# Kernel tuning notes

Hardware: AMD Instinct MI355X
Metric: run time of the kernel (lower is better)

Reference implementation:

```python
import jax, jax.numpy as jnp
import numpy as np

B, S, E, H = 4, 1024, 1024, 16
D = E // H  # head_dim = 64
SCALE = float(np.sqrt(D))


def setup_inputs() -> dict:
    key = jax.random.key(0)
    ks = jax.random.split(key, 12)
    lim = 1.0 / np.sqrt(E)  # torch nn.Linear default init range

    def lin(kw, kb):
        W = jax.random.uniform(kw, (E, E), jnp.float32, -lim, lim)
        b = jax.random.uniform(kb, (E,), jnp.float32, -lim, lim)
        return W, b

    W0, b0 = lin(ks[0], ks[1])
    W1, b1 = lin(ks[2], ks[3])
    W2, b2 = lin(ks[4], ks[5])
    Wv, bv = lin(ks[6], ks[7])
    Wo, bo = lin(ks[8], ks[9])
    A = jax.random.normal(ks[10], (D, D, D), jnp.float32)  # torch.randn core tensor
    x = jax.random.normal(ks[11], (B, S, E), jnp.float32)
    return {"x": x, "W0": W0, "b0": b0, "W1": W1, "b1": b1, "W2": W2, "b2": b2,
            "Wv": Wv, "bv": bv, "Wo": Wo, "bo": bo, "A": A}


def _heads(h):
    # (B,S,E) -> (B,H,S,D)
    return h.reshape(B, S, H, D).transpose(0, 2, 1, 3)


def reference(x, W0, b0, W1, b1, W2, b2, Wv, bv, Wo, bo, A):
    p0 = _heads(x @ W0.T + b0)
    p1 = _heads(x @ W1.T + b1)
    p2 = _heads(x @ W2.T + b2)
    # N=3 multilinear attention score: third projection is contracted over its
    # own sequence index k (faithful to the original einsum construction).
    logits = jnp.einsum('acd,bhia,bhjc,bhkd->bhij', A, p0, p1, p2,
                        optimize=True) / SCALE  # (B,H,S,S)
    attn = jax.nn.softmax(logits, axis=-1)  # dropout inactive (eval / p=0)
    v = _heads(x @ Wv.T + bv)
    values = jnp.einsum('bhij,bhjd->bhid', attn, v)  # (B,H,S,D)
    values = values.transpose(0, 2, 1, 3).reshape(B, S, E)
    out = values @ Wo.T + bo
    return out, attn
```

## Files before the change

kernel.cpp:

```cpp
#include <hip/hip_runtime.h>
#include <hip/hip_bf16.h>
#include <cstddef>

#define B_ 4
#define S_ 1024
#define E_ 1024
#define H_ 16
#define D_ 64
#define BH_ (B_*H_)

typedef __attribute__((ext_vector_type(8))) short short8;
typedef __attribute__((ext_vector_type(4))) float f32x4;
typedef __attribute__((ext_vector_type(4))) unsigned short us4;
typedef unsigned short u16;

__device__ inline u16 f2b(float x) {
    return __builtin_bit_cast(u16, __float2bfloat16(x));
}
__device__ inline float b2f(u16 u) {
    return __bfloat162float(__builtin_bit_cast(__hip_bfloat16, u));
}
__device__ inline void splitf(float x, u16& h, u16& l) {
    h = f2b(x); l = f2b(x - b2f(h));
}

__device__ inline void split_one(const float* __restrict__ in,
                                 u16* __restrict__ oh, u16* __restrict__ ol, int i)
{
    float4 v = ((const float4*)in)[i];
    us4 h, l;
    splitf(v.x, ((u16*)&h)[0], ((u16*)&l)[0]);
    splitf(v.y, ((u16*)&h)[1], ((u16*)&l)[1]);
    splitf(v.z, ((u16*)&h)[2], ((u16*)&l)[2]);
    splitf(v.w, ((u16*)&h)[3], ((u16*)&l)[3]);
    ((us4*)oh)[i] = h;
    ((us4*)ol)[i] = l;
}

__device__ inline void conv_one(const float* __restrict__ in,
                                u16* __restrict__ ob, int i)
{
    float4 v = ((const float4*)in)[i];
    us4 h;
    ((u16*)&h)[0] = f2b(v.x); ((u16*)&h)[1] = f2b(v.y);
    ((u16*)&h)[2] = f2b(v.z); ((u16*)&h)[3] = f2b(v.w);
    ((us4*)ob)[i] = h;
}

__global__ __launch_bounds__(256) void prep(
    const float* __restrict__ x, const float* __restrict__ W0,
    const float* __restrict__ W1, const float* __restrict__ Wv,
    const float* __restrict__ Wo, float* __restrict__ xsum_p,
    u16* __restrict__ xh, u16* __restrict__ xl,
    u16* __restrict__ w0h, u16* __restrict__ w0l,
    u16* __restrict__ w1h, u16* __restrict__ w1l,
    u16* __restrict__ wvb, u16* __restrict__ wob)
{
    int bid = blockIdx.x, tid = threadIdx.x;
    if (bid < 4096) {
        split_one(x, xh, xl, bid * 256 + tid);
    } else if (bid < 5120) {
        split_one(W0, w0h, w0l, (bid - 4096) * 256 + tid);
    } else if (bid < 6144) {
        split_one(W1, w1h, w1l, (bid - 5120) * 256 + tid);
    } else if (bid < 7168) {
        conv_one(Wv, wvb, (bid - 6144) * 256 + tid);
    } else if (bid < 8192) {
        conv_one(Wo, wob, (bid - 7168) * 256 + tid);
    } else {
        int p = bid - 8192;
        int kb = p & 3, b = (p >> 2) & 3, ch = p >> 4;
        int k = kb * 256 + tid;
        const float* base = x + ((size_t)(b * S_ + ch * 64)) * E_ + k;
        float s = 0.f;
#pragma unroll 8
        for (int j = 0; j < 64; ++j) s += base[(size_t)j * E_];
        xsum_p[(ch * 4 + b) * E_ + k] = s;
    }
}

__global__ __launch_bounds__(256) void t2k_M(
    const float* __restrict__ W2, const float* __restrict__ b2v,
    const float* __restrict__ xsum_p, const float* __restrict__ A,
    u16* __restrict__ MTh, u16* __restrict__ MTl)
{
    int h = blockIdx.x, b = blockIdx.y, tid = threadIdx.x;
    __shared__ float xs[1024];
    __shared__ float t2s[64];

#pragma unroll
    for (int j = 0; j < 4; ++j) {
        int k = j * 256 + tid;
        float s = 0.f;
#pragma unroll
        for (int c = 0; c < 16; ++c) s += xsum_p[(c * 4 + b) * E_ + k];
        xs[k] = s;
    }
    __syncthreads();

    int w = tid >> 6, lane = tid & 63;
    for (int nn = w; nn < 64; nn += 4) {
        int n = h * 64 + nn;
        const float* wr = W2 + (size_t)n * E_;
        float s = 0.f;
#pragma unroll
        for (int t = 0; t < 16; ++t) s = fmaf(wr[t * 64 + lane], xs[t * 64 + lane], s);
#pragma unroll
        for (int off = 1; off < 64; off <<= 1) s += __shfl_xor(s, off, 64);
        if (lane == 0) t2s[nn] = s + 1024.0f * b2v[n];
    }
    __syncthreads();

    int bh = b * H_ + h;
    int c = tid & 63;
    int a0 = (tid >> 6) * 16;
    for (int a = a0; a < a0 + 16; ++a) {
        float s = 0.f;
        const float* Ap = A + ((size_t)a * 64 + c) * 64;
#pragma unroll 8
        for (int d = 0; d < 64; ++d) s = fmaf(Ap[d], t2s[d], s);
        u16 hh, ll; splitf(s * 0.125f, hh, ll);
        MTh[(size_t)bh * 4096 + c * 64 + a] = hh;
        MTl[(size_t)bh * 4096 + c * 64 + a] = ll;
    }
}

__device__ void qp1_body(
    const u16* __restrict__ Xh, const u16* __restrict__ Xl,
    const u16* __restrict__ W0h_, const u16* __restrict__ W0l_,
    const u16* __restrict__ W1h_, const u16* __restrict__ W1l_,
    const float* __restrict__ bias0, const float* __restrict__ bias1,
    const u16* __restrict__ MTh, const u16* __restrict__ MTl,
    u16* __restrict__ qh, u16* __restrict__ ql,
    u16* __restrict__ p1h, u16* __restrict__ p1l,
    int bm, int bn, char* smem)
{
    const int K = 1024;
    u16* Xs_h  = (u16*)smem;
    u16* Xs_l  = Xs_h + 128 * 40;
    u16* W0s_h = Xs_l + 128 * 40;
    u16* W0s_l = W0s_h + 64 * 40;
    u16* W1s_h = W0s_l + 64 * 40;
    u16* W1s_l = W1s_h + 64 * 40;
    u16* Cs_h  = (u16*)smem;
    u16* Cs_l  = Cs_h + 128 * 72;

    const int tid = threadIdx.x;
    const int w = tid >> 6, lane = tid & 63;
    const int waveM = w & 1, waveN = w >> 1;
    const int quad = lane >> 4, l16 = lane & 15;

    const int xrow = tid >> 1, xko = (tid & 1) * 16;
    const int wrow = tid >> 2, wko = (tid & 3) * 8;

    const u16* xh_g  = Xh  + (size_t)(bm * 128 + xrow) * K + xko;
    const u16* xl_g  = Xl  + (size_t)(bm * 128 + xrow) * K + xko;
    const u16* w0h_g = W0h_ + (size_t)(bn * 64 + wrow) * K + wko;
    const u16* w0l_g = W0l_ + (size_t)(bn * 64 + wrow) * K + wko;
    const u16* w1h_g = W1h_ + (size_t)(bn * 64 + wrow) * K + wko;
    const u16* w1l_g = W1l_ + (size_t)(bn * 64 + wrow) * K + wko;

    f32x4 acc0[4][2] = {};
    f32x4 acc1[4][2] = {};

    for (int k0 = 0; k0 < K; k0 += 32) {
        uint4 xa = *(const uint4*)(xh_g + k0);
        uint4 xb = *(const uint4*)(xh_g + k0 + 8);
        uint4 xc = *(const uint4*)(xl_g + k0);
        uint4 xd = *(const uint4*)(xl_g + k0 + 8);
        uint4 w0a = *(const uint4*)(w0h_g + k0);
        uint4 w0c = *(const uint4*)(w0l_g + k0);
        uint4 w1a = *(const uint4*)(w1h_g + k0);
        uint4 w1c = *(const uint4*)(w1l_g + k0);
        __syncthreads();
        *(uint4*)&Xs_h[xrow * 40 + xko]     = xa;
        *(uint4*)&Xs_h[xrow * 40 + xko + 8] = xb;
        *(uint4*)&Xs_l[xrow * 40 + xko]     = xc;
        *(uint4*)&Xs_l[xrow * 40 + xko + 8] = xd;
        *(uint4*)&W0s_h[wrow * 40 + wko] = w0a;
        *(uint4*)&W0s_l[wrow * 40 + wko] = w0c;
        *(uint4*)&W1s_h[wrow * 40 + wko] = w1a;
        *(uint4*)&W1s_l[wrow * 40 + wko] = w1c;
        __syncthreads();

        short8 ah[4], al[4], b0h[2], b0l[2], b1h[2], b1l[2];
#pragma unroll
        for (int mt = 0; mt < 4; ++mt) {
            int r = (waveM * 64 + mt * 16 + l16) * 40 + quad * 8;
            ah[mt] = *(short8*)&Xs_h[r];
            al[mt] = *(short8*)&Xs_l[r];
        }
#pragma unroll
        for (int nt = 0; nt < 2; ++nt) {
            int r = (waveN * 32 + nt * 16 + l16) * 40 + quad * 8;
            b0h[nt] = *(short8*)&W0s_h[r];
            b0l[nt] = *(short8*)&W0s_l[r];
            b1h[nt] = *(short8*)&W1s_h[r];
            b1l[nt] = *(short8*)&W1s_l[r];
        }
#pragma unroll
        for (int mt = 0; mt < 4; ++mt)
#pragma unroll
            for (int nt = 0; nt < 2; ++nt) {
                acc0[mt][nt] = __builtin_amdgcn_mfma_f32_16x16x32_bf16(ah[mt], b0h[nt], acc0[mt][nt], 0, 0, 0);
                acc1[mt][nt] = __builtin_amdgcn_mfma_f32_16x16x32_bf16(ah[mt], b1h[nt], acc1[mt][nt], 0, 0, 0);
                acc0[mt][nt] = __builtin_amdgcn_mfma_f32_16x16x32_bf16(ah[mt], b0l[nt], acc0[mt][nt], 0, 0, 0);
                acc1[mt][nt] = __builtin_amdgcn_mfma_f32_16x16x32_bf16(ah[mt], b1l[nt], acc1[mt][nt], 0, 0, 0);
                acc0[mt][nt] = __builtin_amdgcn_mfma_f32_16x16x32_bf16(al[mt], b0h[nt], acc0[mt][nt], 0, 0, 0);
                acc1[mt][nt] = __builtin_amdgcn_mfma_f32_16x16x32_bf16(al[mt], b1h[nt], acc1[mt][nt], 0, 0, 0);
            }
    }

    const int bh = (bm >> 3) * H_ + bn;

#pragma unroll
    for (int mt = 0; mt < 4; ++mt)
#pragma unroll
        for (int nt = 0; nt < 2; ++nt)
#pragma unroll
            for (int r = 0; r < 4; ++r) {
                int m = bm * 128 + waveM * 64 + mt * 16 + quad * 4 + r;
                int n = bn * 64 + waveN * 32 + nt * 16 + l16;
                float val = acc1[mt][nt][r] + bias1[n];
                int s = m & 1023, c = n & 63;
                size_t addr = ((size_t)bh * S_ + s) * 64 + c;
                u16 hh, ll; splitf(val, hh, ll);
                p1h[addr] = hh; p1l[addr] = ll;
            }

    __syncthreads();
#pragma unroll
    for (int mt = 0; mt < 4; ++mt)
#pragma unroll
        for (int nt = 0; nt < 2; ++nt)
#pragma unroll
            for (int r = 0; r < 4; ++r) {
                int i = waveM * 64 + mt * 16 + quad * 4 + r;
                int a = waveN * 32 + nt * 16 + l16;
                float val = acc0[mt][nt][r] + bias0[bn * 64 + a];
                u16 hh, ll; splitf(val, hh, ll);
                Cs_h[i * 72 + a] = hh;
                Cs_l[i * 72 + a] = ll;
            }
    __syncthreads();

    const u16* MTh_b = MTh + (size_t)bh * 4096;
    const u16* MTl_b = MTl + (size_t)bh * 4096;
    f32x4 qacc[4][2] = {};
#pragma unroll
    for (int ch = 0; ch < 2; ++ch) {
        short8 mh[2], ml[2];
#pragma unroll
        for (int nt = 0; nt < 2; ++nt) {
            int c = waveN * 32 + nt * 16 + l16;
            mh[nt] = *(const short8*)&MTh_b[c * 64 + ch * 32 + quad * 8];
            ml[nt] = *(const short8*)&MTl_b[c * 64 + ch * 32 + quad * 8];
        }
#pragma unroll
        for (int mt = 0; mt < 4; ++mt) {
            int rr = (waveM * 64 + mt * 16 + l16) * 72 + ch * 32 + quad * 8;
            short8 ca = *(short8*)&Cs_h[rr];
            short8 cl = *(short8*)&Cs_l[rr];
#pragma unroll
            for (int nt = 0; nt < 2; ++nt) {
                qacc[mt][nt] = __builtin_amdgcn_mfma_f32_16x16x32_bf16(ca, mh[nt], qacc[mt][nt], 0, 0, 0);
                qacc[mt][nt] = __builtin_amdgcn_mfma_f32_16x16x32_bf16(ca, ml[nt], qacc[mt][nt], 0, 0, 0);
                qacc[mt][nt] = __builtin_amdgcn_mfma_f32_16x16x32_bf16(cl, mh[nt], qacc[mt][nt], 0, 0, 0);
            }
        }
    }
#pragma unroll
    for (int mt = 0; mt < 4; ++mt)
#pragma unroll
        for (int nt = 0; nt < 2; ++nt)
#pragma unroll
            for (int r = 0; r < 4; ++r) {
                int s = (bm & 7) * 128 + waveM * 64 + mt * 16 + quad * 4 + r;
                int c = waveN * 32 + nt * 16 + l16;
                size_t addr = ((size_t)bh * S_ + s) * 64 + c;
                u16 hh, ll; splitf(qacc[mt][nt][r], hh, ll);
                qh[addr] = hh; ql[addr] = ll;
            }
}

__device__ void plain128_body(
    const u16* __restrict__ Xb, const u16* __restrict__ Wb,
    const float* __restrict__ bias, u16* __restrict__ outB,
    float* __restrict__ outF, int mode, int bm, int bn, char* smem)
{
    const int K = 1024;
    u16* Xs = (u16*)smem;
    u16* Ws = Xs + 128 * 40;

    const int tid = threadIdx.x;
    const int w = tid >> 6, lane = tid & 63;
    const int waveM = w & 1, waveN = w >> 1;
    const int quad = lane >> 4, l16 = lane & 15;
    const int row = tid >> 1, ko = (tid & 1) * 16;

    const u16* xg = Xb + (size_t)(bm * 128 + row) * K + ko;
    const u16* wg = Wb + (size_t)(bn * 128 + row) * K + ko;

    f32x4 acc[4][4] = {};

    for (int k0 = 0; k0 < K; k0 += 32) {
        uint4 xa = *(const uint4*)(xg + k0);
        uint4 xb = *(const uint4*)(xg + k0 + 8);
        uint4 wa = *(const uint4*)(wg + k0);
        uint4 wb = *(const uint4*)(wg + k0 + 8);
        __syncthreads();
        *(uint4*)&Xs[row * 40 + ko]     = xa;
        *(uint4*)&Xs[row * 40 + ko + 8] = xb;
        *(uint4*)&Ws[row * 40 + ko]     = wa;
        *(uint4*)&Ws[row * 40 + ko + 8] = wb;
        __syncthreads();

        short8 af[4], bf_[4];
#pragma unroll
        for (int mt = 0; mt < 4; ++mt)
            af[mt] = *(short8*)&Xs[(waveM * 64 + mt * 16 + l16) * 40 + quad * 8];
#pragma unroll
        for (int nt = 0; nt < 4; ++nt)
            bf_[nt] = *(short8*)&Ws[(waveN * 64 + nt * 16 + l16) * 40 + quad * 8];
#pragma unroll
        for (int mt = 0; mt < 4; ++mt)
#pragma unroll
            for (int nt = 0; nt < 4; ++nt)
                acc[mt][nt] = __builtin_amdgcn_mfma_f32_16x16x32_bf16(af[mt], bf_[nt], acc[mt][nt], 0, 0, 0);
    }

#pragma unroll
    for (int mt = 0; mt < 4; ++mt)
#pragma unroll
        for (int nt = 0; nt < 4; ++nt)
#pragma unroll
            for (int r = 0; r < 4; ++r) {
                int m = bm * 128 + waveM * 64 + mt * 16 + quad * 4 + r;
                int n = bn * 128 + waveN * 64 + nt * 16 + l16;
                float val = acc[mt][nt][r] + bias[n];
                if (mode == 0) {
                    int b = m >> 10, s = m & 1023, h = n >> 6, c = n & 63;
                    outB[((size_t)((b * H_ + h) * 64 + c)) * S_ + s] = f2b(val);
                } else {
                    outF[(size_t)m * 1024 + n] = val;
                }
            }
}

__global__ __launch_bounds__(256) void gemm_mid(
    const u16* __restrict__ xh, const u16* __restrict__ xl,
    const u16* __restrict__ w0h, const u16* __restrict__ w0l,
    const u16* __restrict__ w1h, const u16* __restrict__ w1l,
    const float* __restrict__ b0, const float* __restrict__ b1,
    const u16* __restrict__ MTh, const u16* __restrict__ MTl,
    u16* __restrict__ qh, u16* __restrict__ ql,
    u16* __restrict__ p1h, u16* __restrict__ p1l,
    const u16* __restrict__ wvb, const float* __restrict__ bv,
    u16* __restrict__ vT)
{
    __shared__ __align__(16) char smem[40960];
    int bid0 = blockIdx.x;
    if (bid0 < 512) {
        int bid = (bid0 & 7) * 64 + (bid0 >> 3);
        qp1_body(xh, xl, w0h, w0l, w1h, w1l, b0, b1, MTh, MTl,
                 qh, ql, p1h, p1l, bid & 31, bid >> 5, smem);
    } else {
        int b2 = bid0 - 512;
        b2 = (b2 & 7) * 32 + (b2 >> 3);
        plain128_body(xh, wvb, bv, vT, nullptr, 0, b2 & 31, b2 >> 5, smem);
    }
}

__global__ __launch_bounds__(256) void gemm_fin(
    const u16* __restrict__ values, const u16* __restrict__ wob,
    const float* __restrict__ bo, float* __restrict__ out)
{
    __shared__ __align__(16) char smem[20480];
    plain128_body(values, wob, bo, nullptr, out, 1, blockIdx.x, blockIdx.y, smem);
}

__global__ __launch_bounds__(512) void logits_softmax_pv(
    const u16* __restrict__ qh, const u16* __restrict__ ql,
    const u16* __restrict__ p1h, const u16* __restrict__ p1l,
    const u16* __restrict__ vT, float* __restrict__ attn,
    u16* __restrict__ values)
{
    int bh = blockIdx.x, i0 = blockIdx.y * 32;
    int b = bh >> 4, h = bh & 15;
    int tid = threadIdx.x, w = tid >> 6, lane = tid & 63;
    int quad = lane >> 4, l16 = lane & 15;
    int wg = w >> 2, wj = w & 3;

    __shared__ __align__(16) char sm[56320];
    u16* qhs  = (u16*)sm;
    u16* qls  = (u16*)(sm + 4608);
    u16* p1hs = (u16*)(sm + 9216);
    u16* p1ls = (u16*)(sm + 27648);
    float* redm = (float*)(sm + 55296);
    float* reds = (float*)(sm + 55808);
    u16* Ps  = (u16*)sm;
    u16* vs_ = (u16*)(sm + 18432);

    {
        int row = tid >> 4, c0 = (tid & 15) * 4;
        size_t g = ((size_t)bh * S_ + i0 + row) * 64 + c0;
        *(us4*)&qhs[row * 72 + c0] = *(const us4*)&qh[g];
        *(us4*)&qls[row * 72 + c0] = *(const us4*)&ql[g];
    }

    const int jl = tid >> 3, c0s = (tid & 7) * 8;
    const size_t gp = ((size_t)bh * S_ + jl) * 64 + c0s;

    uint4 rha = *(const uint4*)&p1h[gp];
    uint4 rla = *(const uint4*)&p1l[gp];
    *(uint4*)&p1hs[jl * 72 + c0s] = rha;
    *(uint4*)&p1ls[jl * 72 + c0s] = rla;
    uint4 rh1 = *(const uint4*)&p1h[gp + 4096];
    uint4 rl1 = *(const uint4*)&p1l[gp + 4096];
    __syncthreads();

    short8 ah[2], al[2];
#pragma unroll
    for (int ch = 0; ch < 2; ++ch) {
        ah[ch] = *(short8*)&qhs[(wg * 16 + l16) * 72 + ch * 32 + quad * 8];
        al[ch] = *(short8*)&qls[(wg * 16 + l16) * 72 + ch * 32 + quad * 8];
    }

    f32x4 L[16];
    for (int t = 0; t < 16; ++t) {
        int cur = t & 1;
        uint4 rh2, rl2;
        if (t < 14) {
            size_t gn = gp + (size_t)(t + 2) * 4096;
            rh2 = *(const uint4*)&p1h[gn];
            rl2 = *(const uint4*)&p1l[gn];
        }
        int jr = wj * 16 + l16;
        const u16* Hb = &p1hs[cur * 4608 + jr * 72];
        const u16* Lb = &p1ls[cur * 4608 + jr * 72];
        short8 bh0 = *(const short8*)(Hb + quad * 8);
        short8 bh1 = *(const short8*)(Hb + 32 + quad * 8);
        short8 bl0 = *(const short8*)(Lb + quad * 8);
        short8 bl1 = *(const short8*)(Lb + 32 + quad * 8);
        f32x4 a = {};
        a = __builtin_amdgcn_mfma_f32_16x16x32_bf16(ah[0], bh0, a, 0, 0, 0);
        a = __builtin_amdgcn_mfma_f32_16x16x32_bf16(ah[1], bh1, a, 0, 0, 0);
        a = __builtin_amdgcn_mfma_f32_16x16x32_bf16(ah[0], bl0, a, 0, 0, 0);
        a = __builtin_amdgcn_mfma_f32_16x16x32_bf16(ah[1], bl1, a, 0, 0, 0);
        a = __builtin_amdgcn_mfma_f32_16x16x32_bf16(al[0], bh0, a, 0, 0, 0);
        a = __builtin_amdgcn_mfma_f32_16x16x32_bf16(al[1], bh1, a, 0, 0, 0);
        L[t] = a;
        if (t < 15) {
            *(uint4*)&p1hs[(1 - cur) * 4608 + jl * 72 + c0s] = rh1;
            *(uint4*)&p1ls[(1 - cur) * 4608 + jl * 72 + c0s] = rl1;
            if (t < 14) { rh1 = rh2; rl1 = rl2; }
            __syncthreads();
        }
    }

    float mrow[4], srow[4];
#pragma unroll
    for (int r = 0; r < 4; ++r) {
        float m = L[0][r];
#pragma unroll
        for (int t = 1; t < 16; ++t) m = fmaxf(m, L[t][r]);
#pragma unroll
        for (int off = 1; off < 16; off <<= 1) m = fmaxf(m, __shfl_xor(m, off, 64));
        mrow[r] = m;
    }
    if (l16 == 0)
#pragma unroll
        for (int r = 0; r < 4; ++r) redm[wj * 32 + wg * 16 + quad * 4 + r] = mrow[r];
    __syncthreads();
#pragma unroll
    for (int r = 0; r < 4; ++r) {
        int rowg = wg * 16 + quad * 4 + r;
        float m = fmaxf(fmaxf(redm[0 * 32 + rowg], redm[1 * 32 + rowg]),
                        fmaxf(redm[2 * 32 + rowg], redm[3 * 32 + rowg]));
        float s = 0.f;
#pragma unroll
        for (int t = 0; t < 16; ++t) { L[t][r] = __expf(L[t][r] - m); s += L[t][r]; }
#pragma unroll
        for (int off = 1; off < 16; off <<= 1) s += __shfl_xor(s, off, 64);
        srow[r] = s;
    }
    if (l16 == 0)
#pragma unroll
        for (int r = 0; r < 4; ++r) reds[wj * 32 + wg * 16 + quad * 4 + r] = srow[r];
    __syncthreads();
#pragma unroll
    for (int r = 0; r < 4; ++r) {
        int rowg = wg * 16 + quad * 4 + r;
        float inv = 1.0f / (reds[0 * 32 + rowg] + reds[1 * 32 + rowg] +
                            reds[2 * 32 + rowg] + reds[3 * 32 + rowg]);
        float* arow = attn + ((size_t)bh * S_ + i0 + rowg) * S_;
#pragma unroll
        for (int t = 0; t < 16; ++t) {
            float p = L[t][r] * inv;
            L[t][r] = p;
            __builtin_nontemporal_store(p, &arow[t * 64 + wj * 16 + l16]);
        }
    }

    const int dv = tid >> 3, jc = (tid & 7) * 8;
    const size_t gv = (size_t)(bh * 64 + dv) * S_;
    uint4 rv0 = *(const uint4*)&vT[gv + jc];
    uint4 rv1 = *(const uint4*)&vT[gv + 64 + jc];

    f32x4 acc_pv = {};
    const int d = wj * 16 + l16;
    for (int tt = 0; tt < 8; ++tt) {
        int cur = tt & 1;
        u16* Pb = Ps + cur * 4608;
        u16* Vb = vs_ + cur * 9216;
#pragma unroll
        for (int r = 0; r < 4; ++r) {
            int pr = (wg * 16 + quad * 4 + r) * 72 + wj * 16 + l16;
            Pb[pr]        = f2b(L[2 * tt][r]);
            Pb[2304 + pr] = f2b(L[2 * tt + 1][r]);
        }
        *(uint4*)&Vb[dv * 72 + jc]        = rv0;
        *(uint4*)&Vb[4608 + dv * 72 + jc] = rv1;
        __syncthreads();
        if (tt < 7) {
            rv0 = *(const uint4*)&vT[gv + (size_t)(2 * tt + 2) * 64 + jc];
            rv1 = *(const uint4*)&vT[gv + (size_t)(2 * tt + 3) * 64 + jc];
        }
#pragma unroll
        for (int tp = 0; tp < 2; ++tp)
#pragma unroll
            for (int cc = 0; cc < 64; cc += 32) {
                short8 af = *(short8*)&Pb[tp * 2304 + (wg * 16 + l16) * 72 + cc + quad * 8];
                short8 bf = *(short8*)&vs_[cur * 9216 + tp * 4608 + d * 72 + cc + quad * 8];
                acc_pv = __builtin_amdgcn_mfma_f32_16x16x32_bf16(af, bf, acc_pv, 0, 0, 0);
            }
    }
#pragma unroll
    for (int r = 0; r < 4; ++r) {
        int i = i0 + wg * 16 + quad * 4 + r;
        values[((size_t)(b * S_ + i)) * E_ + h * 64 + d] = f2b(acc_pv[r]);
    }
}

extern "C" void kernel_launch(void* const* d_in, const int* in_sizes, int n_in,
                              void* d_out, int out_size, void* d_ws, size_t ws_size,
                              hipStream_t stream)
{
    const float* x  = (const float*)d_in[0];
    const float* W0 = (const float*)d_in[1];
    const float* b0 = (const float*)d_in[2];
    const float* W1 = (const float*)d_in[3];
    const float* b1 = (const float*)d_in[4];
    const float* W2 = (const float*)d_in[5];
    const float* b2 = (const float*)d_in[6];
    const float* Wv = (const float*)d_in[7];
    const float* bv = (const float*)d_in[8];
    const float* Wo = (const float*)d_in[9];
    const float* bo = (const float*)d_in[10];
    const float* A  = (const float*)d_in[11];

    float* out  = (float*)d_out;
    float* attn = out + (size_t)B_ * S_ * E_;

    u16* xh  = (u16*)d_ws;
    u16* xl  = xh + 4194304;
    u16* w0h = xl + 4194304;
    u16* w0l = w0h + 1048576;
    u16* w1h = w0l + 1048576;
    u16* w1l = w1h + 1048576;
    u16* p1h = w1l + 1048576;
    u16* p1l = p1h + 4194304;
    u16* qh  = p1l + 4194304;
    u16* ql  = qh + 4194304;
    u16* vT  = ql + 4194304;
    u16* values = vT + 4194304;
    u16* MTh = values + 4194304;
    u16* MTl = MTh + 262144;
    u16* wob = MTl + 262144;
    float* xsum_p = (float*)p1h;
    u16* wvb = values;

    prep<<<8448, 256, 0, stream>>>(x, W0, W1, Wv, Wo, xsum_p,
                                   xh, xl, w0h, w0l, w1h, w1l, wvb, wob);
    t2k_M<<<dim3(16, 4), 256, 0, stream>>>(W2, b2, xsum_p, A, MTh, MTl);

    gemm_mid<<<768, 256, 0, stream>>>(xh, xl, w0h, w0l, w1h, w1l,
                                      b0, b1, MTh, MTl, qh, ql, p1h, p1l,
                                      wvb, bv, vT);

    logits_softmax_pv<<<dim3(64, 32), 512, 0, stream>>>(qh, ql, p1h, p1l, vT, attn, values);

    gemm_fin<<<dim3(32, 8), 256, 0, stream>>>(values, wob, bo, out);
}
```

Measured before the change: 546.3 us.

## Double query rows per block in fused logits-softmax-PV kernel to halve K/V reloads

Each block of the attention kernel now handles 64 query rows instead of 32, with each wave computing two 16-row sub-tiles. The p1 (key-side) and vT tiles streamed through shared memory are shared by twice as many rows, halving their global loads and LDS staging per output. The PV loop is restructured into 16 single-tile steps. In exchange the grid halves to 1024 blocks, register pressure roughly doubles (two 16-entry logit arrays held per thread), and occupancy may drop.

```diff
diff --git a/kernel.cpp b/kernel.cpp
--- a/kernel.cpp
+++ b/kernel.cpp
@@ -385,27 +385,27 @@
     const u16* __restrict__ vT, float* __restrict__ attn,
     u16* __restrict__ values)
 {
-    int bh = blockIdx.x, i0 = blockIdx.y * 32;
+    int bh = blockIdx.x, i0 = blockIdx.y * 64;
     int b = bh >> 4, h = bh & 15;
     int tid = threadIdx.x, w = tid >> 6, lane = tid & 63;
     int quad = lane >> 4, l16 = lane & 15;
     int wg = w >> 2, wj = w & 3;
 
-    __shared__ __align__(16) char sm[56320];
+    __shared__ __align__(16) char sm[57344];
     u16* qhs  = (u16*)sm;
-    u16* qls  = (u16*)(sm + 4608);
-    u16* p1hs = (u16*)(sm + 9216);
-    u16* p1ls = (u16*)(sm + 27648);
+    u16* qls  = (u16*)(sm + 9216);
+    u16* p1hs = (u16*)(sm + 18432);
+    u16* p1ls = (u16*)(sm + 36864);
     float* redm = (float*)(sm + 55296);
-    float* reds = (float*)(sm + 55808);
+    float* reds = (float*)(sm + 56320);
     u16* Ps  = (u16*)sm;
     u16* vs_ = (u16*)(sm + 18432);
 
     {
-        int row = tid >> 4, c0 = (tid & 15) * 4;
+        int row = tid >> 3, c0 = (tid & 7) * 8;
         size_t g = ((size_t)bh * S_ + i0 + row) * 64 + c0;
-        *(us4*)&qhs[row * 72 + c0] = *(const us4*)&qh[g];
-        *(us4*)&qls[row * 72 + c0] = *(const us4*)&ql[g];
+        *(uint4*)&qhs[row * 72 + c0] = *(const uint4*)&qh[g];
+        *(uint4*)&qls[row * 72 + c0] = *(const uint4*)&ql[g];
     }
 
     const int jl = tid >> 3, c0s = (tid & 7) * 8;
@@ -419,14 +419,17 @@
     uint4 rl1 = *(const uint4*)&p1l[gp + 4096];
     __syncthreads();
 
-    short8 ah[2], al[2];
-#pragma unroll
-    for (int ch = 0; ch < 2; ++ch) {
-        ah[ch] = *(short8*)&qhs[(wg * 16 + l16) * 72 + ch * 32 + quad * 8];
-        al[ch] = *(short8*)&qls[(wg * 16 + l16) * 72 + ch * 32 + quad * 8];
-    }
-
-    f32x4 L[16];
+    short8 ah[2][2], al[2][2];
+#pragma unroll
+    for (int rb = 0; rb < 2; ++rb)
+#pragma unroll
+        for (int ch = 0; ch < 2; ++ch) {
+            int row = rb * 32 + wg * 16 + l16;
+            ah[rb][ch] = *(short8*)&qhs[row * 72 + ch * 32 + quad * 8];
+            al[rb][ch] = *(short8*)&qls[row * 72 + ch * 32 + quad * 8];
+        }
+
+    f32x4 L[2][16];
     for (int t = 0; t < 16; ++t) {
         int cur = t & 1;
         uint4 rh2, rl2;
@@ -442,14 +445,17 @@
         short8 bh1 = *(const short8*)(Hb + 32 + quad * 8);
         short8 bl0 = *(const short8*)(Lb + quad * 8);
         short8 bl1 = *(const short8*)(Lb + 32 + quad * 8);
-        f32x4 a = {};
-        a = __builtin_amdgcn_mfma_f32_16x16x32_bf16(ah[0], bh0, a, 0, 0, 0);
-        a = __builtin_amdgcn_mfma_f32_16x16x32_bf16(ah[1], bh1, a, 0, 0, 0);
-        a = __builtin_amdgcn_mfma_f32_16x16x32_bf16(ah[0], bl0, a, 0, 0, 0);
-        a = __builtin_amdgcn_mfma_f32_16x16x32_bf16(ah[1], bl1, a, 0, 0, 0);
-        a = __builtin_amdgcn_mfma_f32_16x16x32_bf16(al[0], bh0, a, 0, 0, 0);
-        a = __builtin_amdgcn_mfma_f32_16x16x32_bf16(al[1], bh1, a, 0, 0, 0);
-        L[t] = a;
+#pragma unroll
+        for (int rb = 0; rb < 2; ++rb) {
+            f32x4 a = {};
+            a = __builtin_amdgcn_mfma_f32_16x16x32_bf16(ah[rb][0], bh0, a, 0, 0, 0);
+            a = __builtin_amdgcn_mfma_f32_16x16x32_bf16(ah[rb][1], bh1, a, 0, 0, 0);
+            a = __builtin_amdgcn_mfma_f32_16x16x32_bf16(ah[rb][0], bl0, a, 0, 0, 0);
+            a = __builtin_amdgcn_mfma_f32_16x16x32_bf16(ah[rb][1], bl1, a, 0, 0, 0);
+            a = __builtin_amdgcn_mfma_f32_16x16x32_bf16(al[rb][0], bh0, a, 0, 0, 0);
+            a = __builtin_amdgcn_mfma_f32_16x16x32_bf16(al[rb][1], bh1, a, 0, 0, 0);
+            L[rb][t] = a;
+        }
         if (t < 15) {
             *(uint4*)&p1hs[(1 - cur) * 4608 + jl * 72 + c0s] = rh1;
             *(uint4*)&p1ls[(1 - cur) * 4608 + jl * 72 + c0s] = rl1;
@@ -458,88 +464,98 @@
         }
     }
 
-    float mrow[4], srow[4];
-#pragma unroll
-    for (int r = 0; r < 4; ++r) {
-        float m = L[0][r];
-#pragma unroll
-        for (int t = 1; t < 16; ++t) m = fmaxf(m, L[t][r]);
-#pragma unroll
-        for (int off = 1; off < 16; off <<= 1) m = fmaxf(m, __shfl_xor(m, off, 64));
-        mrow[r] = m;
-    }
+    float mrow[2][4], srow[2][4];
+#pragma unroll
+    for (int rb = 0; rb < 2; ++rb)
+#pragma unroll
+        for (int r = 0; r < 4; ++r) {
+            float m = L[rb][0][r];
+#pragma unroll
+            for (int t = 1; t < 16; ++t) m = fmaxf(m, L[rb][t][r]);
+#pragma unroll
+            for (int off = 1; off < 16; off <<= 1) m = fmaxf(m, __shfl_xor(m, off, 64));
+            mrow[rb][r] = m;
+        }
     if (l16 == 0)
 #pragma unroll
-        for (int r = 0; r < 4; ++r) redm[wj * 32 + wg * 16 + quad * 4 + r] = mrow[r];
+        for (int rb = 0; rb < 2; ++rb)
+#pragma unroll
+            for (int r = 0; r < 4; ++r)
+                redm[wj * 64 + rb * 32 + wg * 16 + quad * 4 + r] = mrow[rb][r];
     __syncthreads();
 #pragma unroll
-    for (int r = 0; r < 4; ++r) {
-        int rowg = wg * 16 + quad * 4 + r;
-        float m = fmaxf(fmaxf(redm[0 * 32 + rowg], redm[1 * 32 + rowg]),
-                        fmaxf(redm[2 * 32 + rowg], redm[3 * 32 + rowg]));
-        float s = 0.f;
-#pragma unroll
-        for (int t = 0; t < 16; ++t) { L[t][r] = __expf(L[t][r] - m); s += L[t][r]; }
-#pragma unroll
-        for (int off = 1; off < 16; off <<= 1) s += __shfl_xor(s, off, 64);
-        srow[r] = s;
-    }
+    for (int rb = 0; rb < 2; ++rb)
+#pragma unroll
+        for (int r = 0; r < 4; ++r) {
+            int row64 = rb * 32 + wg * 16 + quad * 4 + r;
+            float m = fmaxf(fmaxf(redm[0 * 64 + row64], redm[1 * 64 + row64]),
+                            fmaxf(redm[2 * 64 + row64], redm[3 * 64 + row64]));
+            float s = 0.f;
+#pragma unroll
+            for (int t = 0; t < 16; ++t) { L[rb][t][r] = __expf(L[rb][t][r] - m); s += L[rb][t][r]; }
+#pragma unroll
+            for (int off = 1; off < 16; off <<= 1) s += __shfl_xor(s, off, 64);
+            srow[rb][r] = s;
+        }
     if (l16 == 0)
 #pragma unroll
-        for (int r = 0; r < 4; ++r) reds[wj * 32 + wg * 16 + quad * 4 + r] = srow[r];
+        for (int rb = 0; rb < 2; ++rb)
+#pragma unroll
+            for (int r = 0; r < 4; ++r)
+                reds[wj * 64 + rb * 32 + wg * 16 + quad * 4 + r] = srow[rb][r];
     __syncthreads();
 #pragma unroll
-    for (int r = 0; r < 4; ++r) {
-        int rowg = wg * 16 + quad * 4 + r;
-        float inv = 1.0f / (reds[0 * 32 + rowg] + reds[1 * 32 + rowg] +
-                            reds[2 * 32 + rowg] + reds[3 * 32 + rowg]);
-        float* arow = attn + ((size_t)bh * S_ + i0 + rowg) * S_;
-#pragma unroll
-        for (int t = 0; t < 16; ++t) {
-            float p = L[t][r] * inv;
-            L[t][r] = p;
-            __builtin_nontemporal_store(p, &arow[t * 64 + wj * 16 + l16]);
-        }
-    }
+    for (int rb = 0; rb < 2; ++rb)
+#pragma unroll
+        for (int r = 0; r < 4; ++r) {
+            int row64 = rb * 32 + wg * 16 + quad * 4 + r;
+            float inv = 1.0f / (reds[0 * 64 + row64] + reds[1 * 64 + row64] +
+                                reds[2 * 64 + row64] + reds[3 * 64 + row64]);
+            float* arow = attn + ((size_t)bh * S_ + i0 + row64) * S_;
+#pragma unroll
+            for (int t = 0; t < 16; ++t) {
+                float p = L[rb][t][r] * inv;
+                L[rb][t][r] = p;
+                __builtin_nontemporal_store(p, &arow[t * 64 + wj * 16 + l16]);
+            }
+        }
 
     const int dv = tid >> 3, jc = (tid & 7) * 8;
     const size_t gv = (size_t)(bh * 64 + dv) * S_;
-    uint4 rv0 = *(const uint4*)&vT[gv + jc];
-    uint4 rv1 = *(const uint4*)&vT[gv + 64 + jc];
-
-    f32x4 acc_pv = {};
+    uint4 rv = *(const uint4*)&vT[gv + jc];
+
+    f32x4 acc_pv[2] = {};
     const int d = wj * 16 + l16;
-    for (int tt = 0; tt < 8; ++tt) {
-        int cur = tt & 1;
+    for (int t = 0; t < 16; ++t) {
+        int cur = t & 1;
         u16* Pb = Ps + cur * 4608;
-        u16* Vb = vs_ + cur * 9216;
+        u16* Vb = vs_ + cur * 4608;
+#pragma unroll
+        for (int rb = 0; rb < 2; ++rb)
+#pragma unroll
+            for (int r = 0; r < 4; ++r) {
+                int row64 = rb * 32 + wg * 16 + quad * 4 + r;
+                Pb[row64 * 72 + wj * 16 + l16] = f2b(L[rb][t][r]);
+            }
+        *(uint4*)&Vb[dv * 72 + jc] = rv;
+        __syncthreads();
+        if (t < 15) rv = *(const uint4*)&vT[gv + (size_t)(t + 1) * 64 + jc];
+#pragma unroll
+        for (int rb = 0; rb < 2; ++rb)
+#pragma unroll
+            for (int cc = 0; cc < 64; cc += 32) {
+                short8 af = *(short8*)&Pb[(rb * 32 + wg * 16 + l16) * 72 + cc + quad * 8];
+                short8 bf = *(short8*)&Vb[d * 72 + cc + quad * 8];
+                acc_pv[rb] = __builtin_amdgcn_mfma_f32_16x16x32_bf16(af, bf, acc_pv[rb], 0, 0, 0);
+            }
+    }
+#pragma unroll
+    for (int rb = 0; rb < 2; ++rb)
 #pragma unroll
         for (int r = 0; r < 4; ++r) {
-            int pr = (wg * 16 + quad * 4 + r) * 72 + wj * 16 + l16;
-            Pb[pr]        = f2b(L[2 * tt][r]);
-            Pb[2304 + pr] = f2b(L[2 * tt + 1][r]);
-        }
-        *(uint4*)&Vb[dv * 72 + jc]        = rv0;
-        *(uint4*)&Vb[4608 + dv * 72 + jc] = rv1;
-        __syncthreads();
-        if (tt < 7) {
-            rv0 = *(const uint4*)&vT[gv + (size_t)(2 * tt + 2) * 64 + jc];
-            rv1 = *(const uint4*)&vT[gv + (size_t)(2 * tt + 3) * 64 + jc];
-        }
-#pragma unroll
-        for (int tp = 0; tp < 2; ++tp)
-#pragma unroll
-            for (int cc = 0; cc < 64; cc += 32) {
-                short8 af = *(short8*)&Pb[tp * 2304 + (wg * 16 + l16) * 72 + cc + quad * 8];
-                short8 bf = *(short8*)&vs_[cur * 9216 + tp * 4608 + d * 72 + cc + quad * 8];
-                acc_pv = __builtin_amdgcn_mfma_f32_16x16x32_bf16(af, bf, acc_pv, 0, 0, 0);
-            }
-    }
-#pragma unroll
-    for (int r = 0; r < 4; ++r) {
-        int i = i0 + wg * 16 + quad * 4 + r;
-        values[((size_t)(b * S_ + i)) * E_ + h * 64 + d] = f2b(acc_pv[r]);
-    }
+            int i = i0 + rb * 32 + wg * 16 + quad * 4 + r;
+            values[((size_t)(b * S_ + i)) * E_ + h * 64 + d] = f2b(acc_pv[rb][r]);
+        }
 }
 
 extern "C" void kernel_launch(void* const* d_in, const int* in_sizes, int n_in,
@@ -588,7 +604,7 @@
                                       b0, b1, MTh, MTl, qh, ql, p1h, p1l,
                                       wvb, bv, vT);
 
-    logits_softmax_pv<<<dim3(64, 32), 512, 0, stream>>>(qh, ql, p1h, p1l, vT, attn, values);
+    logits_softmax_pv<<<dim3(64, 16), 512, 0, stream>>>(qh, ql, p1h, p1l, vT, attn, values);
 
     gemm_fin<<<dim3(32, 8), 256, 0, stream>>>(values, wob, bo, out);
 }
```

Result: slower. 574.4 us (+5.1%).
